# Kernel optimization log

Measured on AMD Instinct MI355X. Metric: run time of the kernel, lower is better.

## Reference

```python
import jax, jax.numpy as jnp
import numpy as np

D_MODEL, D_K, D_FF, N = 1024, 128, 4096, 8192

def _linear_params(key, fan_in, fan_out):
    # mimic torch nn.Linear default init (uniform +/- 1/sqrt(fan_in))
    k1, k2 = jax.random.split(key)
    bound = 1.0 / np.sqrt(fan_in)
    W = jax.random.uniform(k1, (fan_out, fan_in), jnp.float32, -bound, bound)
    b = jax.random.uniform(k2, (fan_out,), jnp.float32, -bound, bound)
    return W, b

def setup_inputs() -> dict:
    key = jax.random.key(0)
    ks = jax.random.split(key, 7)
    x = jax.random.normal(ks[0], (N, D_MODEL), jnp.float32)
    Wq, bq = _linear_params(ks[1], D_MODEL, D_K)
    Wk, bk = _linear_params(ks[2], D_MODEL, D_K)
    Wv, bv = _linear_params(ks[3], D_MODEL, D_K)
    Wp, bp = _linear_params(ks[4], D_K, D_MODEL)
    W1, b1 = _linear_params(ks[5], D_MODEL, D_FF)
    W2, b2 = _linear_params(ks[6], D_FF, D_MODEL)
    return {"x": x, "Wq": Wq, "bq": bq, "Wk": Wk, "bk": bk, "Wv": Wv, "bv": bv,
            "Wp": Wp, "bp": bp, "W1": W1, "b1": b1, "W2": W2, "b2": b2}

def reference(x, Wq, bq, Wk, bk, Wv, bv, Wp, bp, W1, b1, W2, b2):
    # projections (torch Linear: x @ W.T + b)
    Q = x @ Wq.T + bq            # [n, d_k]
    K = x @ Wk.T + bk            # [n, d_k]
    V = x @ Wv.T + bv            # [n, d_k]
    # linear attention, original evaluation order: (Q @ K^T) @ V
    attn = Q @ K.T               # [n, n]
    context = attn @ V           # [n, d_k]
    out = context @ Wp.T + bp    # [n, d_model]
    x = x + out                  # residual 1
    h = jax.nn.relu(x @ W1.T + b1)  # [n, d_ff]
    return x + (h @ W2.T + b2)   # residual 2
```

## Files before the change

### kernel.cpp

```cpp
#include <hip/hip_runtime.h>


#define MROWS 8192
#define DMODEL 1024
#define DK 128
#define DFF 4096

typedef __attribute__((ext_vector_type(8))) __bf16 bf16x8;
typedef __attribute__((ext_vector_type(4))) float f32x4;

#define BAR()    asm volatile("s_barrier" ::: "memory")
#define WAITV(n) asm volatile("s_waitcnt vmcnt(" #n ")" ::: "memory")
#define GLOAD(src, dst) __builtin_amdgcn_global_load_lds( \
    (const __attribute__((address_space(1))) void*)(src), \
    (__attribute__((address_space(3))) void*)(dst), 16, 0, 0)

__global__ __launch_bounds__(256) void cast_f32_bf16(
    const float* __restrict__ src, __bf16* __restrict__ dst, int n8)
{
    for (int i = blockIdx.x * blockDim.x + threadIdx.x; i < n8;
         i += gridDim.x * blockDim.x) {
        const float4 a = reinterpret_cast<const float4*>(src)[2 * i];
        const float4 b = reinterpret_cast<const float4*>(src)[2 * i + 1];
        bf16x8 o;
        o[0] = (__bf16)a.x; o[1] = (__bf16)a.y; o[2] = (__bf16)a.z; o[3] = (__bf16)a.w;
        o[4] = (__bf16)b.x; o[5] = (__bf16)b.y; o[6] = (__bf16)b.z; o[7] = (__bf16)b.w;
        reinterpret_cast<bf16x8*>(dst)[i] = o;
    }
}

__global__ void pack_bias3(const float* __restrict__ a, const float* __restrict__ b,
                           const float* __restrict__ c, float* __restrict__ o)
{
    const int t = threadIdx.x;
    o[t] = a[t]; o[128 + t] = b[t]; o[256 + t] = c[t];
}

__global__ __launch_bounds__(256) void ffn2_reduce(
    float* __restrict__ y, const __bf16* __restrict__ P0,
    const __bf16* __restrict__ P1, const float* __restrict__ b2, int n8)
{
    for (int i = blockIdx.x * blockDim.x + threadIdx.x; i < n8;
         i += gridDim.x * blockDim.x) {
        const int col0 = (i << 3) & (DMODEL - 1);
        const float4 ba = *reinterpret_cast<const float4*>(&b2[col0]);
        const float4 bb = *reinterpret_cast<const float4*>(&b2[col0 + 4]);
        float4 o0 = reinterpret_cast<const float4*>(y)[2 * i];
        float4 o1 = reinterpret_cast<const float4*>(y)[2 * i + 1];
        const bf16x8 p0 = reinterpret_cast<const bf16x8*>(P0)[i];
        const bf16x8 p1 = reinterpret_cast<const bf16x8*>(P1)[i];
        o0.x += (float)p0[0] + (float)p1[0] + ba.x;
        o0.y += (float)p0[1] + (float)p1[1] + ba.y;
        o0.z += (float)p0[2] + (float)p1[2] + ba.z;
        o0.w += (float)p0[3] + (float)p1[3] + ba.w;
        o1.x += (float)p0[4] + (float)p1[4] + bb.x;
        o1.y += (float)p0[5] + (float)p1[5] + bb.y;
        o1.z += (float)p0[6] + (float)p1[6] + bb.z;
        o1.w += (float)p0[7] + (float)p1[7] + bb.w;
        reinterpret_cast<float4*>(y)[2 * i]     = o0;
        reinterpret_cast<float4*>(y)[2 * i + 1] = o1;
    }
}

template<bool RELU, bool RESID, bool BIAS, bool OUTBF, bool DUAL>
__global__ __launch_bounds__(256) void gemm128(
    const __bf16* __restrict__ A, int lda,
    const __bf16* __restrict__ W,
    const float* __restrict__ bias,
    const float* __restrict__ resid,
    void* __restrict__ Cout, __bf16* __restrict__ Cbf, int ldc, int K)
{
    constexpr int BK = 32;
    __shared__ __bf16 As[128 * BK];
    __shared__ __bf16 Bs[128 * BK];

    const int tid  = threadIdx.x;
    const int lane = tid & 63;
    const int w    = tid >> 6;
    const int wm   = w >> 1;
    const int wn   = w & 1;
    const int fr   = lane & 15;
    const int fq   = lane >> 4;

    const long row0 = (long)blockIdx.y * 128;
    const long col0 = (long)blockIdx.x * 128;

    const int sr = (w << 4) + (lane >> 2);
    const int sc = (lane & 3) << 3;

    const __bf16* gA0 = A + (row0 + sr) * (long)lda + sc;
    const __bf16* gA1 = A + (row0 + 64 + sr) * (long)lda + sc;
    const __bf16* gW0 = W + (col0 + sr) * (long)K + sc;
    const __bf16* gW1 = W + (col0 + 64 + sr) * (long)K + sc;

    __bf16* lA0 = &As[(w << 4) * BK];
    __bf16* lA1 = &As[((w << 4) + 64) * BK];
    __bf16* lB0 = &Bs[(w << 4) * BK];
    __bf16* lB1 = &Bs[((w << 4) + 64) * BK];

    f32x4 acc[4][4] = {};

    for (int k0 = 0; k0 < K; k0 += BK) {
        GLOAD(gA0 + k0, lA0);
        GLOAD(gA1 + k0, lA1);
        GLOAD(gW0 + k0, lB0);
        GLOAD(gW1 + k0, lB1);
        __syncthreads();

        bf16x8 af[4], bfr[4];
        #pragma unroll
        for (int m = 0; m < 4; m++)
            af[m] = *reinterpret_cast<const bf16x8*>(
                &As[(wm * 64 + m * 16 + fr) * BK + fq * 8]);
        #pragma unroll
        for (int n = 0; n < 4; n++)
            bfr[n] = *reinterpret_cast<const bf16x8*>(
                &Bs[(wn * 64 + n * 16 + fr) * BK + fq * 8]);

        #pragma unroll
        for (int m = 0; m < 4; m++)
            #pragma unroll
            for (int n = 0; n < 4; n++)
                acc[m][n] = __builtin_amdgcn_mfma_f32_16x16x32_bf16(
                    af[m], bfr[n], acc[m][n], 0, 0, 0);
        __syncthreads();
    }

    #pragma unroll
    for (int n = 0; n < 4; n++) {
        const long c = col0 + wn * 64 + n * 16 + fr;
        float bc = 0.0f;
        if constexpr (BIAS) bc = bias[c];
        #pragma unroll
        for (int m = 0; m < 4; m++) {
            #pragma unroll
            for (int j = 0; j < 4; j++) {
                const long r = row0 + wm * 64 + m * 16 + fq * 4 + j;
                float v = acc[m][n][j];
                if constexpr (BIAS)  v += bc;
                if constexpr (RESID) v += resid[r * ldc + c];
                if constexpr (RELU)  v = fmaxf(v, 0.0f);
                if constexpr (OUTBF) ((__bf16*)Cout)[r * ldc + c] = (__bf16)v;
                else                 ((float*)Cout)[r * ldc + c] = v;
                if constexpr (DUAL)  Cbf[r * ldc + c] = (__bf16)v;
            }
        }
    }
}

template<bool RELU, bool RESID, bool BIAS, bool OUTBF>
__global__ __launch_bounds__(512, 2) void gemm256p(
    const __bf16* __restrict__ A, int lda,
    const __bf16* __restrict__ W, int ldw,
    const float* __restrict__ bias,
    const float* __restrict__ resid,
    void* __restrict__ Cout, long sstride, int ldc,
    int klen, int nb, int nbx)
{
    __shared__ char lds[8][16384];

    const int bid = blockIdx.x;
    const int sid = bid / nb;
    const int ib  = bid % nb;
    const int chunk = nb >> 3;
    const int swz   = (ib & 7) * chunk + (ib >> 3);
    const int bx    = swz % nbx;
    const int by    = swz / nbx;

    const long row0 = (long)by * 256;
    const long col0 = (long)bx * 256;

    const __bf16* Ash = A + (long)sid * klen;
    const __bf16* Wsh = W + (long)sid * klen;

    const int tid  = threadIdx.x;
    const int lane = tid & 63;
    const int w    = tid >> 6;
    const int wm   = w >> 2;
    const int wn   = w & 3;
    const int fr   = lane & 15;
    const int fq   = lane >> 4;

    const int srow8 = lane >> 3;
    const int scole = ((lane & 7) ^ srow8) << 3;
    const __bf16* gA = Ash + (row0 + w * 8 + srow8) * (long)lda + scole;
    const __bf16* gB = Wsh + (col0 + w * 8 + srow8) * (long)ldw + scole;

    char* ldsc = &lds[0][0];
    const int nt = klen >> 6;

    auto stage = [&](int u, int j) {
        if (u >= nt) return;
        char* dst = ldsc + (((u & 1) << 2 | j) << 14) + (w << 10);
        if (j < 2) {
            const __bf16* s = gB + ((long)j * 128) * (long)ldw + (long)u * 64;
            GLOAD(s, dst);
            GLOAD(s + 64 * (long)ldw, dst + 8192);
        } else {
            const __bf16* s = gA + ((long)(j - 2) * 128) * (long)lda + (long)u * 64;
            GLOAD(s, dst);
            GLOAD(s + 64 * (long)lda, dst + 8192);
        }
    };

    const int rb0 = fr * 128 + ((fq * 16) ^ ((fr & 7) << 4));
    const int rb1 = fr * 128 + ((64 + fq * 16) ^ ((fr & 7) << 4));

    f32x4 acc[8][4] = {};

    stage(0, 0); stage(0, 1); stage(0, 2); stage(0, 3);
    stage(1, 0); stage(1, 1); stage(1, 2); stage(1, 3);
    WAITV(8);
    BAR();

    for (int t = 0; t < nt; ++t) {
        const char* base = ldsc + ((t & 1) << 16);
        const char* pB = base + ((wn >> 1) << 14) + ((wn & 1) << 13);
        const char* pA = base + ((2 + wm) << 14);

        bf16x8 a[8][2], bb[4][2];

        #pragma unroll
        for (int n = 0; n < 4; n++) {
            bb[n][0] = *reinterpret_cast<const bf16x8*>(pB + rb0 + n * 2048);
            bb[n][1] = *reinterpret_cast<const bf16x8*>(pB + rb1 + n * 2048);
        }
        #pragma unroll
        for (int m = 0; m < 2; m++) {
            a[m][0] = *reinterpret_cast<const bf16x8*>(pA + rb0 + m * 2048);
            a[m][1] = *reinterpret_cast<const bf16x8*>(pA + rb1 + m * 2048);
        }
        BAR();
        __builtin_amdgcn_s_setprio(1);
        #pragma unroll
        for (int m = 0; m < 2; m++)
            #pragma unroll
            for (int n = 0; n < 4; n++) {
                acc[m][n] = __builtin_amdgcn_mfma_f32_16x16x32_bf16(
                    a[m][0], bb[n][0], acc[m][n], 0, 0, 0);
                acc[m][n] = __builtin_amdgcn_mfma_f32_16x16x32_bf16(
                    a[m][1], bb[n][1], acc[m][n], 0, 0, 0);
            }
        __builtin_amdgcn_s_setprio(0);
        BAR();

        #pragma unroll
        for (int m = 2; m < 6; m++) {
            a[m][0] = *reinterpret_cast<const bf16x8*>(pA + rb0 + m * 2048);
            a[m][1] = *reinterpret_cast<const bf16x8*>(pA + rb1 + m * 2048);
        }
        stage(t + 2, 0);
        stage(t + 2, 1);
        BAR();
        __builtin_amdgcn_s_setprio(1);
        #pragma unroll
        for (int m = 2; m < 4; m++)
            #pragma unroll
            for (int n = 0; n < 4; n++) {
                acc[m][n] = __builtin_amdgcn_mfma_f32_16x16x32_bf16(
                    a[m][0], bb[n][0], acc[m][n], 0, 0, 0);
                acc[m][n] = __builtin_amdgcn_mfma_f32_16x16x32_bf16(
                    a[m][1], bb[n][1], acc[m][n], 0, 0, 0);
            }
        __builtin_amdgcn_s_setprio(0);
        BAR();

        #pragma unroll
        for (int m = 6; m < 8; m++) {
            a[m][0] = *reinterpret_cast<const bf16x8*>(pA + rb0 + m * 2048);
            a[m][1] = *reinterpret_cast<const bf16x8*>(pA + rb1 + m * 2048);
        }
        BAR();
        __builtin_amdgcn_s_setprio(1);
        #pragma unroll
        for (int m = 4; m < 6; m++)
            #pragma unroll
            for (int n = 0; n < 4; n++) {
                acc[m][n] = __builtin_amdgcn_mfma_f32_16x16x32_bf16(
                    a[m][0], bb[n][0], acc[m][n], 0, 0, 0);
                acc[m][n] = __builtin_amdgcn_mfma_f32_16x16x32_bf16(
                    a[m][1], bb[n][1], acc[m][n], 0, 0, 0);
            }
        __builtin_amdgcn_s_setprio(0);
        BAR();

        stage(t + 2, 2);
        stage(t + 2, 3);
        BAR();
        __builtin_amdgcn_s_setprio(1);
        #pragma unroll
        for (int m = 6; m < 8; m++)
            #pragma unroll
            for (int n = 0; n < 4; n++) {
                acc[m][n] = __builtin_amdgcn_mfma_f32_16x16x32_bf16(
                    a[m][0], bb[n][0], acc[m][n], 0, 0, 0);
                acc[m][n] = __builtin_amdgcn_mfma_f32_16x16x32_bf16(
                    a[m][1], bb[n][1], acc[m][n], 0, 0, 0);
            }
        __builtin_amdgcn_s_setprio(0);

        if (t + 2 < nt)      { WAITV(8); }
        else if (t + 1 < nt) { WAITV(0); }
        BAR();
    }

    __bf16* Cb = (__bf16*)Cout + (long)sid * sstride;
    float*  Cf = (float*)Cout;
    #pragma unroll
    for (int n = 0; n < 4; n++) {
        const long c = col0 + wn * 64 + n * 16 + fr;
        float bc = 0.0f;
        if constexpr (BIAS) bc = bias[c];
        #pragma unroll
        for (int m = 0; m < 8; m++) {
            #pragma unroll
            for (int j = 0; j < 4; j++) {
                const long r = row0 + wm * 128 + m * 16 + fq * 4 + j;
                float v = acc[m][n][j];
                if constexpr (BIAS)  v += bc;
                if constexpr (RESID) v += resid[r * ldc + c];
                if constexpr (RELU)  v = fmaxf(v, 0.0f);
                if constexpr (OUTBF) Cb[r * ldc + c] = (__bf16)v;
                else                 Cf[r * ldc + c] = v;
            }
        }
    }
}

__global__ __launch_bounds__(256) void ktv_partial(
    const __bf16* __restrict__ Kp, const __bf16* __restrict__ Vp,
    int ld, float* __restrict__ part)
{
    __shared__ float ks[32][DK];
    __shared__ float vs[32][DK];
    const int tid = threadIdx.x;
    const int ti  = tid >> 4;
    const int tj  = tid & 15;
    float acc[8][8] = {};
    const long base = (long)blockIdx.x * 128;

    for (int n0 = 0; n0 < 128; n0 += 32) {
        for (int t = tid; t < 512; t += 256) {
            const int r  = t >> 4;
            const int cc = (t & 15) << 3;
            const bf16x8 k8 = *reinterpret_cast<const bf16x8*>(
                &Kp[(base + n0 + r) * (long)ld + cc]);
            const bf16x8 v8 = *reinterpret_cast<const bf16x8*>(
                &Vp[(base + n0 + r) * (long)ld + cc]);
            #pragma unroll
            for (int u = 0; u < 8; u++) {
                ks[r][cc + u] = (float)k8[u];
                vs[r][cc + u] = (float)v8[u];
            }
        }
        __syncthreads();
        for (int n = 0; n < 32; n++) {
            float kk[8], vv[8];
            #pragma unroll
            for (int i = 0; i < 8; i++) kk[i] = ks[n][(ti << 3) + i];
            #pragma unroll
            for (int j = 0; j < 8; j++) vv[j] = vs[n][(tj << 3) + j];
            #pragma unroll
            for (int i = 0; i < 8; i++)
                #pragma unroll
                for (int j = 0; j < 8; j++)
                    acc[i][j] = fmaf(kk[i], vv[j], acc[i][j]);
        }
        __syncthreads();
    }

    float* dst = &part[(long)blockIdx.x * (DK * DK)];
    #pragma unroll
    for (int i = 0; i < 8; i++) {
        const int ig = (ti << 3) + i;
        *reinterpret_cast<float4*>(&dst[ig * DK + (tj << 3)]) =
            make_float4(acc[i][0], acc[i][1], acc[i][2], acc[i][3]);
        *reinterpret_cast<float4*>(&dst[ig * DK + (tj << 3) + 4]) =
            make_float4(acc[i][4], acc[i][5], acc[i][6], acc[i][7]);
    }
}

__global__ __launch_bounds__(256) void ktv_reduce(
    const float* __restrict__ part, __bf16* __restrict__ ktvT)
{
    const int t = blockIdx.x * 256 + threadIdx.x;
    const int i = t >> 7;
    const int j = t & 127;
    float s = 0.0f;
    for (int b = 0; b < 64; b++) s += part[(long)b * (DK * DK) + t];
    ktvT[j * DK + i] = (__bf16)s;
}

extern "C" void kernel_launch(void* const* d_in, const int* in_sizes, int n_in,
                              void* d_out, int out_size, void* d_ws, size_t ws_size,
                              hipStream_t stream) {
    const float* x  = (const float*)d_in[0];
    const float* Wq = (const float*)d_in[1];
    const float* bq = (const float*)d_in[2];
    const float* Wk = (const float*)d_in[3];
    const float* bk = (const float*)d_in[4];
    const float* Wv = (const float*)d_in[5];
    const float* bv = (const float*)d_in[6];
    const float* Wp = (const float*)d_in[7];
    const float* bp = (const float*)d_in[8];
    const float* W1 = (const float*)d_in[9];
    const float* b1 = (const float*)d_in[10];
    const float* W2 = (const float*)d_in[11];
    const float* b2 = (const float*)d_in[12];
    float* out = (float*)d_out;

    char* ws = (char*)d_ws;
    const size_t MB = 1ull << 20;
    __bf16* xb    = (__bf16*)(ws);
    __bf16* P0    = (__bf16*)(ws);
    __bf16* P1    = P0 + (long)MROWS * DMODEL;
    __bf16* x2b   = (__bf16*)(ws +  34 * MB);
    __bf16* Hb    = (__bf16*)(ws +  51 * MB);
    __bf16* QKVb  = (__bf16*)(ws + 119 * MB);
    __bf16* W1b   = (__bf16*)(ws + 126 * MB);
    __bf16* W2b   = (__bf16*)(ws + 135 * MB);
    __bf16* Wqkvb = (__bf16*)(ws + 144 * MB);
    __bf16* Wpb   = (__bf16*)(ws + 145 * MB);
    float*  Part  = (float*) (ws + 146 * MB);
    __bf16* KtvTb = (__bf16*)(ws + 151 * MB);
    __bf16* Ctxb  = (__bf16*)(ws + 152 * MB);
    float*  bqkvf = (float*) (ws + 155 * MB);

    const dim3 blk(256);

    cast_f32_bf16<<<2048, blk, 0, stream>>>(x,  xb,           MROWS * DMODEL / 8);
    cast_f32_bf16<<<64,   blk, 0, stream>>>(Wq, Wqkvb,        DK * DMODEL / 8);
    cast_f32_bf16<<<64,   blk, 0, stream>>>(Wk, Wqkvb + DK * DMODEL,     DK * DMODEL / 8);
    cast_f32_bf16<<<64,   blk, 0, stream>>>(Wv, Wqkvb + 2 * DK * DMODEL, DK * DMODEL / 8);
    cast_f32_bf16<<<64,   blk, 0, stream>>>(Wp, Wpb,          DMODEL * DK / 8);
    cast_f32_bf16<<<1024, blk, 0, stream>>>(W1, W1b,          DFF * DMODEL / 8);
    cast_f32_bf16<<<1024, blk, 0, stream>>>(W2, W2b,          DMODEL * DFF / 8);
    pack_bias3<<<1, 128, 0, stream>>>(bq, bk, bv, bqkvf);

    gemm128<false,false,true,true,false><<<dim3(3, 64), blk, 0, stream>>>(
        xb, DMODEL, Wqkvb, bqkvf, nullptr, QKVb, nullptr, 3 * DK, DMODEL);

    ktv_partial<<<64, blk, 0, stream>>>(QKVb + DK, QKVb + 2 * DK, 3 * DK, Part);
    ktv_reduce <<<64, blk, 0, stream>>>(Part, KtvTb);

    gemm128<false,false,false,true,false><<<dim3(1, 64), blk, 0, stream>>>(
        QKVb, 3 * DK, KtvTb, nullptr, nullptr, Ctxb, nullptr, DK, DK);

    gemm128<false,true,true,false,true><<<dim3(8, 64), blk, 0, stream>>>(
        Ctxb, DK, Wpb, bp, x, out, x2b, DMODEL, DK);

    gemm256p<true,false,true,true><<<512, 512, 0, stream>>>(
        x2b, DMODEL, W1b, DMODEL, b1, nullptr, Hb, 0, DFF,
        DMODEL, 512, DFF / 256);

    gemm256p<false,false,false,true><<<256, 512, 0, stream>>>(
        Hb, DFF, W2b, DFF, nullptr, nullptr, P0,
        (long)MROWS * DMODEL, DMODEL, DFF / 2, 128, DMODEL / 256);

    ffn2_reduce<<<2048, blk, 0, stream>>>(out, P0, P1, b2, MROWS * DMODEL / 8);
}
```

Measured before the change: 265.7 us.

## Software-pipeline LDS fragment reads across tiles with double-buffered B registers

Restructures the 256x256 GEMM main loop so that LDS fragment reads for the next A quarter, and for the next tile's B and first A quarter, are issued before the MFMA block that runs in the same phase. B fragments alternate between two register sets, and the loop is unrolled by two tiles. Global staging is spread across four phases, with the vmcnt and lgkmcnt waits adjusted to match. The intent is to hide LDS read latency behind MFMAs and drop the separate read-only phase. The epilogue loop order also changes so bias values are hoisted and stores iterate over columns innermost. Costs are higher register pressure under launch_bounds(512,2). The two-tile unroll assumes nt is even.

Result: slower. 305.6 us (+15.0%).

```diff
diff --git a/kernel.cpp b/kernel.cpp
--- a/kernel.cpp
+++ b/kernel.cpp
@@ -11,6 +11,7 @@
 
 #define BAR()    asm volatile("s_barrier" ::: "memory")
 #define WAITV(n) asm volatile("s_waitcnt vmcnt(" #n ")" ::: "memory")
+#define LGKM0()  asm volatile("s_waitcnt lgkmcnt(0)" ::: "memory")
 #define GLOAD(src, dst) __builtin_amdgcn_global_load_lds( \
     (const __attribute__((address_space(1))) void*)(src), \
     (__attribute__((address_space(3))) void*)(dst), 16, 0, 0)
@@ -126,18 +127,19 @@
         __syncthreads();
     }
 
+    float bc[4];
     #pragma unroll
-    for (int n = 0; n < 4; n++) {
-        const long c = col0 + wn * 64 + n * 16 + fr;
-        float bc = 0.0f;
-        if constexpr (BIAS) bc = bias[c];
+    for (int n = 0; n < 4; n++)
+        bc[n] = BIAS ? bias[col0 + wn * 64 + n * 16 + fr] : 0.0f;
+    #pragma unroll
+    for (int m = 0; m < 4; m++) {
         #pragma unroll
-        for (int m = 0; m < 4; m++) {
-            #pragma unroll
-            for (int j = 0; j < 4; j++) {
-                const long r = row0 + wm * 64 + m * 16 + fq * 4 + j;
-                float v = acc[m][n][j];
-                if constexpr (BIAS)  v += bc;
+        for (int j = 0; j < 4; j++) {
+            const long r = row0 + wm * 64 + m * 16 + fq * 4 + j;
+            #pragma unroll
+            for (int n = 0; n < 4; n++) {
+                const long c = col0 + wn * 64 + n * 16 + fr;
+                float v = acc[m][n][j] + bc[n];
                 if constexpr (RESID) v += resid[r * ldc + c];
                 if constexpr (RELU)  v = fmaxf(v, 0.0f);
                 if constexpr (OUTBF) ((__bf16*)Cout)[r * ldc + c] = (__bf16)v;
@@ -147,6 +149,69 @@
         }
     }
 }
+
+#define LD8(p) (*reinterpret_cast<const bf16x8*>(p))
+
+#define READ_AQ(q, mb, pa)                         \
+    q[0][0] = LD8((pa) + rb0 + (mb) * 2048);       \
+    q[0][1] = LD8((pa) + rb1 + (mb) * 2048);       \
+    q[1][0] = LD8((pa) + rb0 + ((mb) + 1) * 2048); \
+    q[1][1] = LD8((pa) + rb1 + ((mb) + 1) * 2048);
+
+#define READ_B(bset, pb)                           \
+    _Pragma("unroll")                              \
+    for (int n = 0; n < 4; n++) {                  \
+        bset[n][0] = LD8((pb) + rb0 + n * 2048);   \
+        bset[n][1] = LD8((pb) + rb1 + n * 2048);   \
+    }
+
+#define MFMA_Q(q, bset, mb)                                                   \
+    _Pragma("unroll")                                                         \
+    for (int i = 0; i < 2; i++)                                               \
+        _Pragma("unroll")                                                     \
+        for (int n = 0; n < 4; n++) {                                         \
+            acc[(mb) + i][n] = __builtin_amdgcn_mfma_f32_16x16x32_bf16(       \
+                q[i][0], bset[n][0], acc[(mb) + i][n], 0, 0, 0);              \
+            acc[(mb) + i][n] = __builtin_amdgcn_mfma_f32_16x16x32_bf16(       \
+                q[i][1], bset[n][1], acc[(mb) + i][n], 0, 0, 0);              \
+        }
+
+#define TILE(t, BCUR, BNXT)                                                   \
+  {                                                                           \
+    const char* pA  = ldsc + (((t) & 1) << 16) + ((2 + wm) << 14);            \
+    const char* pAn = ldsc + ((((t) + 1) & 1) << 16) + ((2 + wm) << 14);      \
+    const char* pBn = ldsc + ((((t) + 1) & 1) << 16) +                        \
+                      ((wn >> 1) << 14) + ((wn & 1) << 13);                   \
+                        \
+    READ_AQ(qY, 2, pA); stage((t) + 2, 0);                                    \
+    BAR();                                                                    \
+    __builtin_amdgcn_s_setprio(1); MFMA_Q(qX, BCUR, 0);                       \
+    __builtin_amdgcn_s_setprio(0);                                            \
+    BAR();                                                                    \
+                                 \
+    READ_AQ(qX, 4, pA); stage((t) + 2, 1);                                    \
+    BAR();                                                                    \
+    __builtin_amdgcn_s_setprio(1); MFMA_Q(qY, BCUR, 2);                       \
+    __builtin_amdgcn_s_setprio(0);                                            \
+    BAR();                                                                    \
+             \
+    READ_AQ(qY, 6, pA); stage((t) + 2, 2);                                    \
+    BAR();                                                                    \
+    __builtin_amdgcn_s_setprio(1); MFMA_Q(qX, BCUR, 4);                       \
+    __builtin_amdgcn_s_setprio(0);                                            \
+    if ((t) + 2 < nt)      { WAITV(6); }                                      \
+    else if ((t) + 1 < nt) { WAITV(0); }                                      \
+    LGKM0();                                                                  \
+    BAR();                                                                    \
+                 \
+    if ((t) + 1 < nt) { READ_B(BNXT, pBn); READ_AQ(qX, 0, pAn); }             \
+    stage((t) + 2, 3);                                                        \
+    BAR();                                                                    \
+    __builtin_amdgcn_s_setprio(1); MFMA_Q(qY, BCUR, 6);                       \
+    __builtin_amdgcn_s_setprio(0);                                            \
+    LGKM0();                                                                  \
+    BAR();                                                                    \
+  }
 
 template<bool RELU, bool RESID, bool BIAS, bool OUTBF>
 __global__ __launch_bounds__(512, 2) void gemm256p(
@@ -207,117 +272,41 @@
     const int rb1 = fr * 128 + ((64 + fq * 16) ^ ((fr & 7) << 4));
 
     f32x4 acc[8][4] = {};
+    bf16x8 bE[4][2], bO[4][2], qX[2][2], qY[2][2];
 
     stage(0, 0); stage(0, 1); stage(0, 2); stage(0, 3);
     stage(1, 0); stage(1, 1); stage(1, 2); stage(1, 3);
     WAITV(8);
     BAR();
-
-    for (int t = 0; t < nt; ++t) {
-        const char* base = ldsc + ((t & 1) << 16);
-        const char* pB = base + ((wn >> 1) << 14) + ((wn & 1) << 13);
-        const char* pA = base + ((2 + wm) << 14);
-
-        bf16x8 a[8][2], bb[4][2];
-
-        #pragma unroll
-        for (int n = 0; n < 4; n++) {
-            bb[n][0] = *reinterpret_cast<const bf16x8*>(pB + rb0 + n * 2048);
-            bb[n][1] = *reinterpret_cast<const bf16x8*>(pB + rb1 + n * 2048);
-        }
-        #pragma unroll
-        for (int m = 0; m < 2; m++) {
-            a[m][0] = *reinterpret_cast<const bf16x8*>(pA + rb0 + m * 2048);
-            a[m][1] = *reinterpret_cast<const bf16x8*>(pA + rb1 + m * 2048);
-        }
-        BAR();
-        __builtin_amdgcn_s_setprio(1);
-        #pragma unroll
-        for (int m = 0; m < 2; m++)
-            #pragma unroll
-            for (int n = 0; n < 4; n++) {
-                acc[m][n] = __builtin_amdgcn_mfma_f32_16x16x32_bf16(
-                    a[m][0], bb[n][0], acc[m][n], 0, 0, 0);
-                acc[m][n] = __builtin_amdgcn_mfma_f32_16x16x32_bf16(
-                    a[m][1], bb[n][1], acc[m][n], 0, 0, 0);
-            }
-        __builtin_amdgcn_s_setprio(0);
-        BAR();
-
-        #pragma unroll
-        for (int m = 2; m < 6; m++) {
-            a[m][0] = *reinterpret_cast<const bf16x8*>(pA + rb0 + m * 2048);
-            a[m][1] = *reinterpret_cast<const bf16x8*>(pA + rb1 + m * 2048);
-        }
-        stage(t + 2, 0);
-        stage(t + 2, 1);
-        BAR();
-        __builtin_amdgcn_s_setprio(1);
-        #pragma unroll
-        for (int m = 2; m < 4; m++)
-            #pragma unroll
-            for (int n = 0; n < 4; n++) {
-                acc[m][n] = __builtin_amdgcn_mfma_f32_16x16x32_bf16(
-                    a[m][0], bb[n][0], acc[m][n], 0, 0, 0);
-                acc[m][n] = __builtin_amdgcn_mfma_f32_16x16x32_bf16(
-                    a[m][1], bb[n][1], acc[m][n], 0, 0, 0);
-            }
-        __builtin_amdgcn_s_setprio(0);
-        BAR();
-
-        #pragma unroll
-        for (int m = 6; m < 8; m++) {
-            a[m][0] = *reinterpret_cast<const bf16x8*>(pA + rb0 + m * 2048);
-            a[m][1] = *reinterpret_cast<const bf16x8*>(pA + rb1 + m * 2048);
-        }
-        BAR();
-        __builtin_amdgcn_s_setprio(1);
-        #pragma unroll
-        for (int m = 4; m < 6; m++)
-            #pragma unroll
-            for (int n = 0; n < 4; n++) {
-                acc[m][n] = __builtin_amdgcn_mfma_f32_16x16x32_bf16(
-                    a[m][0], bb[n][0], acc[m][n], 0, 0, 0);
-                acc[m][n] = __builtin_amdgcn_mfma_f32_16x16x32_bf16(
-                    a[m][1], bb[n][1], acc[m][n], 0, 0, 0);
-            }
-        __builtin_amdgcn_s_setprio(0);
-        BAR();
-
-        stage(t + 2, 2);
-        stage(t + 2, 3);
-        BAR();
-        __builtin_amdgcn_s_setprio(1);
-        #pragma unroll
-        for (int m = 6; m < 8; m++)
-            #pragma unroll
-            for (int n = 0; n < 4; n++) {
-                acc[m][n] = __builtin_amdgcn_mfma_f32_16x16x32_bf16(
-                    a[m][0], bb[n][0], acc[m][n], 0, 0, 0);
-                acc[m][n] = __builtin_amdgcn_mfma_f32_16x16x32_bf16(
-                    a[m][1], bb[n][1], acc[m][n], 0, 0, 0);
-            }
-        __builtin_amdgcn_s_setprio(0);
-
-        if (t + 2 < nt)      { WAITV(8); }
-        else if (t + 1 < nt) { WAITV(0); }
-        BAR();
+    {
+        const char* pB0 = ldsc + ((wn >> 1) << 14) + ((wn & 1) << 13);
+        const char* pA0 = ldsc + ((2 + wm) << 14);
+        READ_B(bE, pB0);
+        READ_AQ(qX, 0, pA0);
+    }
+    LGKM0();
+    BAR();
+
+    for (int tt = 0; tt < nt; tt += 2) {
+        TILE(tt,     bE, bO)
+        TILE(tt + 1, bO, bE)
     }
 
     __bf16* Cb = (__bf16*)Cout + (long)sid * sstride;
     float*  Cf = (float*)Cout;
+    float bc[4];
     #pragma unroll
-    for (int n = 0; n < 4; n++) {
-        const long c = col0 + wn * 64 + n * 16 + fr;
-        float bc = 0.0f;
-        if constexpr (BIAS) bc = bias[c];
+    for (int n = 0; n < 4; n++)
+        bc[n] = BIAS ? bias[col0 + wn * 64 + n * 16 + fr] : 0.0f;
+    #pragma unroll
+    for (int m = 0; m < 8; m++) {
         #pragma unroll
-        for (int m = 0; m < 8; m++) {
-            #pragma unroll
-            for (int j = 0; j < 4; j++) {
-                const long r = row0 + wm * 128 + m * 16 + fq * 4 + j;
-                float v = acc[m][n][j];
-                if constexpr (BIAS)  v += bc;
+        for (int j = 0; j < 4; j++) {
+            const long r = row0 + wm * 128 + m * 16 + fq * 4 + j;
+            #pragma unroll
+            for (int n = 0; n < 4; n++) {
+                const long c = col0 + wn * 64 + n * 16 + fr;
+                float v = acc[m][n][j] + bc[n];
                 if constexpr (RESID) v += resid[r * ldc + c];
                 if constexpr (RELU)  v = fmaxf(v, 0.0f);
                 if constexpr (OUTBF) Cb[r * ldc + c] = (__bf16)v;
```
